# Performance work log

Measured on AMD Instinct MI355X. Metric: run time of the kernel, lower is better.

## Reference

```python
import jax, jax.numpy as jnp
import numpy as np
from jax import lax

B, N, C, NP, NS, H, L = 2, 16384, 256, 2048, 32, 4, 2
DFF = 2 * C
RADIUS = 1.0
EPS = 1e-5


def setup_inputs() -> dict:
    key = jax.random.key(0)
    ks = jax.random.split(key, 12)
    s = 0.02
    f32 = jnp.float32
    return {
        "xyz": jax.random.normal(ks[0], (B, N, 3), f32),
        "features": jax.random.normal(ks[1], (B, C, N), f32),
        # positional encoding: Conv1x1(3->C/2)+BN(eval)+ReLU, Conv1x1(C/2->C)
        "pe1_w": jax.random.normal(ks[2], (C // 2, 3), f32) * s,
        "pe1_b": jnp.zeros((C // 2,), f32),
        "bn_g": jnp.ones((C // 2,), f32),
        "bn_b": jnp.zeros((C // 2,), f32),
        "bn_m": jnp.zeros((C // 2,), f32),
        "bn_v": jnp.ones((C // 2,), f32),
        "pe2_w": jax.random.normal(ks[3], (C, C // 2), f32) * s,
        "pe2_b": jnp.zeros((C,), f32),
        # L pre-norm transformer encoder layers (stacked on leading dim)
        "ipw": jax.random.normal(ks[4], (L, 3 * C, C), f32) * s,
        "ipb": jnp.zeros((L, 3 * C), f32),
        "opw": jax.random.normal(ks[5], (L, C, C), f32) * s,
        "opb": jnp.zeros((L, C), f32),
        "ln1s": jnp.ones((L, C), f32), "ln1b": jnp.zeros((L, C), f32),
        "ln2s": jnp.ones((L, C), f32), "ln2b": jnp.zeros((L, C), f32),
        "fc1w": jax.random.normal(ks[6], (L, DFF, C), f32) * s,
        "fc1b": jnp.zeros((L, DFF), f32),
        "fc2w": jax.random.normal(ks[7], (L, C, DFF), f32) * s,
        "fc2b": jnp.zeros((L, C), f32),
    }


def _fps(xyz, npoint):
    # D-FPS starting from point 0 (pointnet2 convention). xyz: [B,N,3]
    b, n, _ = xyz.shape

    def step(carry, _):
        dists, far = carry
        centroid = jnp.take_along_axis(xyz, far[:, None, None], axis=1)  # [B,1,3]
        d = jnp.sum((xyz - centroid) ** 2, -1)
        dists = jnp.minimum(dists, d)
        return (dists, jnp.argmax(dists, -1).astype(jnp.int32)), far

    init = (jnp.full((b, n), 1e10, jnp.float32), jnp.zeros((b,), jnp.int32))
    _, idx = lax.scan(step, init, None, length=npoint)
    return idx.T  # [B, npoint]


def _ball_query(xyz, new_xyz, radius, ns):
    # first <=ns points within radius, padded with the first hit. [B,NP,NS]
    n = xyz.shape[1]
    d2 = jnp.sum((new_xyz[:, :, None, :] - xyz[:, None, :, :]) ** 2, -1)  # [B,NP,N]
    scores = jnp.where(d2 < radius * radius, jnp.arange(n, dtype=jnp.int32), n)
    svals = jnp.sort(scores, axis=-1)[..., :ns]
    order = jnp.argsort(scores, axis=-1)[..., :ns].astype(jnp.int32)
    valid = svals < n
    return jnp.where(valid, order, order[..., :1])


def _ln(x, s, b):
    m = jnp.mean(x, -1, keepdims=True)
    v = jnp.var(x, -1, keepdims=True)
    return (x - m) * lax.rsqrt(v + EPS) * s + b


def _mha(x, w, bias, ow, ob):
    # x: [S, Bn, D] (seq-first, like nn.MultiheadAttention)
    S, Bn, D = x.shape
    hd = D // H
    qkv = x @ w.T + bias
    q, k, v = jnp.split(qkv, 3, -1)
    rs = lambda t: t.reshape(S, Bn, H, hd).transpose(1, 2, 0, 3)  # [Bn,H,S,hd]
    q, k, v = rs(q), rs(k), rs(v)
    att = jax.nn.softmax(jnp.einsum('bhqd,bhkd->bhqk', q, k) * (1.0 / np.sqrt(hd)), -1)
    o = jnp.einsum('bhqk,bhkd->bhqd', att, v).transpose(2, 0, 1, 3).reshape(S, Bn, D)
    return o @ ow.T + ob


def reference(xyz, features, pe1_w, pe1_b, bn_g, bn_b, bn_m, bn_v, pe2_w, pe2_b,
              ipw, ipb, opw, opb, ln1s, ln1b, ln2s, ln2b, fc1w, fc1b, fc2w, fc2b):
    # --- sample + group ---
    fps_idx = _fps(lax.stop_gradient(xyz), NP)                       # [B,NP]
    new_xyz = jnp.take_along_axis(xyz, fps_idx[:, :, None], axis=1)  # [B,NP,3]
    idx = _ball_query(lax.stop_gradient(xyz), lax.stop_gradient(new_xyz), RADIUS, NS)
    g_xyz = jax.vmap(lambda p, i: p[i])(xyz, idx) - new_xyz[:, :, None, :]  # [B,NP,NS,3]
    g_xyz = g_xyz.transpose(0, 3, 1, 2)                              # [B,3,NP,NS]
    g_feat = jax.vmap(lambda f, i: f[:, i])(features, idx)           # [B,C,NP,NS]
    # --- positional encoding (conv1x1 + BN(eval) + ReLU, conv1x1) ---
    h = jnp.einsum('oc,bcps->bops', pe1_w, g_xyz) + pe1_b[None, :, None, None]
    h = (h - bn_m[None, :, None, None]) * lax.rsqrt(bn_v + EPS)[None, :, None, None]
    h = jax.nn.relu(h * bn_g[None, :, None, None] + bn_b[None, :, None, None])
    pe = jnp.einsum('oc,bcps->bops', pe2_w, h) + pe2_b[None, :, None, None]
    x = g_feat + pe                                                  # [B,C,NP,NS]
    # --- local transformer over each neighborhood (seq len = NS) ---
    x = x.transpose(0, 2, 1, 3).reshape(B * NP, C, NS).transpose(2, 0, 1)  # [NS,B*NP,C]
    for l in range(L):
        x = _ln(x, ln1s[l], ln1b[l])
        x = x + _mha(x, ipw[l], ipb[l], opw[l], opb[l])
        x = _ln(x, ln2s[l], ln2b[l])
        x = x + jax.nn.relu(x @ fc1w[l].T + fc1b[l]) @ fc2w[l].T + fc2b[l]
    tf = x.transpose(1, 2, 0).reshape(B, NP, C, NS).transpose(0, 2, 1, 3)  # [B,C,NP,NS]
    Lf = NP * NS

    def scat(feat_b, tf_b, idx_b):
        idx_f = idx_b.reshape(-1)          # [Lf]
        ff = tf_b.reshape(C, -1)           # [C,Lf]
        pos = jnp.arange(Lf, dtype=jnp.int32)
        first = jax.ops.segment_min(pos, idx_f, num_segments=N)  # [N], maxint if absent
        valid = first < Lf
        safe = jnp.where(valid, first, 0)
        return jnp.where(valid[None, :], ff[:, safe], feat_b)    # [C,N]

    out = jax.vmap(scat)(features, tf, idx)  # [B,C,N]
    return out.transpose(0, 2, 1)            # [B,N,C]
```

## Files before the change

### kernel.cpp

```cpp
#include <hip/hip_runtime.h>

#define NB 2
#define NN 16384
#define NC 256
#define NPp 2048
#define NSs 32
#define NH 4
#define HDh 64
#define NL 2
#define NDFF 512
#define LFv (NPp*NSs)
#define LNEPS 1e-5f
#define NBLK 256
#define NTHR 512
#define NW 8

typedef short s16x8 __attribute__((ext_vector_type(8)));
typedef float f32x4 __attribute__((ext_vector_type(4)));
typedef float f32x2 __attribute__((ext_vector_type(2)));
typedef unsigned short u16;
typedef unsigned long long u64;

struct CtlBlock { int ctr1; int ctr2; int bar; };

__device__ __forceinline__ u16 f2bf(float f){
  unsigned u = __float_as_uint(f);
  u += 0x7fffu + ((u>>16)&1u);
  return (u16)(u>>16);
}

__device__ __forceinline__ f32x4 mfma16(s16x8 a, s16x8 b, f32x4 c){
  return __builtin_amdgcn_mfma_f32_16x16x32_bf16(a, b, c, 0, 0, 0);
}

__device__ __forceinline__ f32x2 pk_add(f32x2 a, f32x2 b){
  f32x2 d; asm("v_pk_add_f32 %0, %1, %2" : "=v"(d) : "v"(a), "v"(b)); return d;
}
__device__ __forceinline__ f32x2 pk_mul(f32x2 a, f32x2 b){
  f32x2 d; asm("v_pk_mul_f32 %0, %1, %2" : "=v"(d) : "v"(a), "v"(b)); return d;
}

#define DPP_FMAX(v, ctrl) do { \
  int _iv = __float_as_int(v); \
  int _sh = __builtin_amdgcn_update_dpp(_iv, _iv, (ctrl), 0xF, 0xF, false); \
  (v) = fmaxf((v), __int_as_float(_sh)); \
} while(0)

#define DPP_IMIN(v, ctrl) do { \
  int _sh = __builtin_amdgcn_update_dpp((v), (v), (ctrl), 0xF, 0xF, false); \
  (v) = (_sh < (v)) ? _sh : (v); \
} while(0)

struct SMem {
  u64  masks[256];
  u64  keybuf[4];
  float wvc[2][NW][4];
  float cxbuf[8][4];
  float xs[32][260];
  u16  xn[32][264];
  u16  qb[32][776];
  u16  pb[NH][32][40];
  int  idx_sh[32];
  float gx_sh[32][3];
  int  misc[16];
  int  win[32];
};

__global__ void k_prep(const float* __restrict__ ipw, const float* __restrict__ opw,
                       const float* __restrict__ fc1w, const float* __restrict__ fc2w,
                       const float* __restrict__ pe2w,
                       const float* __restrict__ bng, const float* __restrict__ bnb,
                       const float* __restrict__ bnm, const float* __restrict__ bnv,
                       u16* ipwb, u16* opwb, u16* fc1wb, u16* fc2wb, u16* pe2wb,
                       float* bnsc, float* bnsh, int* first, int* rdy, CtlBlock* ctl){
  const int i0 = blockIdx.x*blockDim.x + threadIdx.x;
  const int stride = gridDim.x*blockDim.x;
  for (int i=i0; i<NL*768*NC; i+=stride) ipwb[i] = f2bf(ipw[i]);
  for (int i=i0; i<NL*NC*NC; i+=stride)  opwb[i] = f2bf(opw[i]);
  for (int i=i0; i<NL*NDFF*NC; i+=stride) fc1wb[i] = f2bf(fc1w[i]);
  for (int i=i0; i<NL*NC*NDFF; i+=stride) fc2wb[i] = f2bf(fc2w[i]);
  for (int i=i0; i<NC*128; i+=stride)    pe2wb[i] = f2bf(pe2w[i]);
  for (int i=i0; i<NB*NN; i+=stride)     first[i] = LFv;
  for (int i=i0; i<NB*NPp; i+=stride)    rdy[i] = 0;
  for (int i=i0; i<128; i+=stride){
    float sc = bng[i]*rsqrtf(bnv[i]+LNEPS);
    bnsc[i] = sc; bnsh[i] = bnb[i] - bnm[i]*sc;
  }
  if (i0 == 0){ ctl->ctr1 = 0; ctl->ctr2 = 0; ctl->bar = 0; }
}

__global__ __launch_bounds__(256) void k_featT(const float* __restrict__ feat,
                                               float* __restrict__ featT){
  __shared__ float T[32][33];
  const int b = blockIdx.y;
  const int n0 = blockIdx.x*32;
  const int t = threadIdx.x;
  const int tn = t & 31, tc = t >> 5;
  for (int cb=0; cb<NC; cb+=32){
    #pragma unroll
    for (int i=0;i<32;i+=8)
      T[tc+i][tn] = feat[((size_t)b*NC + cb+tc+i)*NN + n0+tn];
    __syncthreads();
    #pragma unroll
    for (int i=0;i<32;i+=8)
      featT[((size_t)b*NN + n0+tc+i)*NC + cb+tn] = T[tn][tc+i];
    __syncthreads();
  }
}

#define SELC(S) case S: scx = px2[(S)>>1][(S)&1]; scy = py2[(S)>>1][(S)&1]; scz = pz2[(S)>>1][(S)&1]; break;

__device__ void fps_run(int b, const float* __restrict__ xyz, u64* __restrict__ cx2,
                        int* __restrict__ rdy, SMem& sm){
#pragma clang fp contract(off)
  const int t = threadIdx.x;
  const int lane = t & 63, wid = t >> 6;
  const float* xb = xyz + (size_t)b*NN*3;
  f32x2 px2[16], py2[16], pz2[16], dd2[16];
  #pragma unroll
  for (int m=0;m<16;m++){
    int i0 = t + (2*m)*NTHR, i1 = t + (2*m+1)*NTHR;
    px2[m] = f32x2{xb[i0*3],   xb[i1*3]};
    py2[m] = f32x2{xb[i0*3+1], xb[i1*3+1]};
    pz2[m] = f32x2{xb[i0*3+2], xb[i1*3+2]};
    dd2[m] = f32x2{1e10f, 1e10f};
  }
  if (t < 4) sm.keybuf[t] = 0ull;
  float ncx, ncy, ncz;
  {
    float wx = xb[0], wy = xb[1], wz = xb[2];
    ncx=-wx; ncy=-wy; ncz=-wz;
    if (t==0){ sm.cxbuf[0][0]=wx; sm.cxbuf[0][1]=wy; sm.cxbuf[0][2]=wz; }
  }
  __syncthreads();
  for (int step=1; step<NPp; ++step){
    const f32x2 ncx2={ncx,ncx}, ncy2={ncy,ncy}, ncz2={ncz,ncz};
    float bestv = -1.f;
    #pragma unroll
    for (int m=0;m<16;m++){
      f32x2 dx = pk_add(px2[m], ncx2);
      f32x2 dy = pk_add(py2[m], ncy2);
      f32x2 dz = pk_add(pz2[m], ncz2);
      f32x2 s  = pk_add(pk_add(pk_mul(dx,dx), pk_mul(dy,dy)), pk_mul(dz,dz));
      dd2[m].x = fminf(dd2[m].x, s.x);
      dd2[m].y = fminf(dd2[m].y, s.y);
      bestv = fmaxf(fmaxf(bestv, dd2[m].x), dd2[m].y);
    }
    float M = bestv;
    DPP_FMAX(M, 0x111); DPP_FMAX(M, 0x112); DPP_FMAX(M, 0x114); DPP_FMAX(M, 0x118);
    DPP_FMAX(M, 0x142); DPP_FMAX(M, 0x143);
    const int Mi = __builtin_amdgcn_readlane(__float_as_int(M), 63);
    const float Ms = __int_as_float(Mi);
    int li = 0x7fffffff;
    #pragma unroll
    for (int m=15;m>=0;m--){
      if (dd2[m].y == Ms) li = t + (2*m+1)*NTHR;
      if (dd2[m].x == Ms) li = t + (2*m)*NTHR;
    }
    DPP_IMIN(li, 0x111); DPP_IMIN(li, 0x112); DPP_IMIN(li, 0x114); DPP_IMIN(li, 0x118);
    DPP_IMIN(li, 0x142); DPP_IMIN(li, 0x143);
    const int li63 = __builtin_amdgcn_readlane(li, 63);
    const int kb = step & 3, cb = step & 1;
    if (lane==0){
      u64 key = ((u64)(unsigned)Mi << 32) | (unsigned)(0x7fffffff - li63);
      atomicMax(&sm.keybuf[kb], key);
    }
    {
      const int slot = li63 >> 9;
      float scx=0.f, scy=0.f, scz=0.f;
      switch(slot){
        SELC(0) SELC(1) SELC(2) SELC(3) SELC(4) SELC(5) SELC(6) SELC(7)
        SELC(8) SELC(9) SELC(10) SELC(11) SELC(12) SELC(13) SELC(14) SELC(15)
        SELC(16) SELC(17) SELC(18) SELC(19) SELC(20) SELC(21) SELC(22) SELC(23)
        SELC(24) SELC(25) SELC(26) SELC(27) SELC(28) SELC(29) SELC(30) SELC(31)
        default: break;
      }
      if (t == (li63 & (NTHR-1))){
        sm.wvc[cb][wid][0]=scx; sm.wvc[cb][wid][1]=scy; sm.wvc[cb][wid][2]=scz;
      }
    }
    __syncthreads();
    const u64 kk = sm.keybuf[kb];
    const int widx = 0x7fffffff - (int)(unsigned)(kk & 0xffffffffull);
    const int wv = (widx & (NTHR-1)) >> 6;
    const float bx = sm.wvc[cb][wv][0];
    const float by = sm.wvc[cb][wv][1];
    const float bz = sm.wvc[cb][wv][2];
    ncx=-bx; ncy=-by; ncz=-bz;
    if (t==0){
      sm.cxbuf[step & 7][0]=bx; sm.cxbuf[step & 7][1]=by; sm.cxbuf[step & 7][2]=bz;
      sm.keybuf[(step+2) & 3] = 0ull;
      if ((step & 7) == 7){
        int s0 = step - 7;
        #pragma unroll
        for (int j=0;j<8;j++){
          float fx=sm.cxbuf[j][0], fy=sm.cxbuf[j][1], fz=sm.cxbuf[j][2];
          u64 lo = ((u64)__float_as_uint(fy) << 32) | __float_as_uint(fx);
          u64 hi = (u64)__float_as_uint(fz);
          size_t pb2 = (size_t)(b*NPp + s0 + j)*2;
          __hip_atomic_store(&cx2[pb2],   lo, __ATOMIC_RELAXED, __HIP_MEMORY_SCOPE_AGENT);
          __hip_atomic_store(&cx2[pb2+1], hi, __ATOMIC_RELAXED, __HIP_MEMORY_SCOPE_AGENT);
        }
        asm volatile("s_waitcnt vmcnt(0)" ::: "memory");
        #pragma unroll
        for (int j=0;j<8;j++)
          __hip_atomic_store(&rdy[b*NPp + s0 + j], 1, __ATOMIC_RELAXED, __HIP_MEMORY_SCOPE_AGENT);
      }
    }
  }
}

__device__ void seq_ballq(const float* __restrict__ xb, float cx, float cy, float cz,
                          SMem& sm, int t, int lane, int wid){
#pragma clang fp contract(off)
  for (int it=0; it<32; ++it){
    int cid = wid*32 + it;
    int i = cid*64 + lane;
    float dx=xb[i*3]-cx, dy=xb[i*3+1]-cy, dz=xb[i*3+2]-cz;
    float d2=(dx*dx+dy*dy)+dz*dz;
    u64 m = __ballot(d2 < 1.0f);
    if (lane==0) sm.masks[cid] = m;
  }
  __syncthreads();
  if (wid==0){
    u64 mk[4]; int cnt=0;
    #pragma unroll
    for (int j=0;j<4;j++){ mk[j]=sm.masks[lane*4+j]; cnt += __popcll(mk[j]); }
    int inc = cnt;
    #pragma unroll
    for (int ofs=1; ofs<64; ofs<<=1){
      int v = __shfl_up(inc, ofs);
      if (lane >= ofs) inc += v;
    }
    int r = inc - cnt;
    int tot = __shfl(inc, 63);
    #pragma unroll
    for (int j=0;j<4;j++){
      u64 msk = mk[j];
      int base = (lane*4+j)*64;
      while (msk && r < NSs){
        int bpos = __ffsll(msk)-1;
        sm.idx_sh[r] = base + bpos;
        msk &= msk-1;
        ++r;
      }
      if (r >= NSs) break;
    }
    int cc = tot < NSs ? tot : NSs;
    int pv = (tot > 0) ? sm.idx_sh[0] : 0;
    if (lane < NSs && lane >= cc) sm.idx_sh[lane] = pv;
  }
  __syncthreads();
}

__device__ __forceinline__ void ln_block512(SMem& sm, const float* __restrict__ s_,
                                            const float* __restrict__ b_, int t){
  const int s = t >> 4, j = t & 15;
  float v[16];
  float sum = 0.f;
  #pragma unroll
  for (int k=0;k<16;k++){ v[k]=sm.xs[s][j*16+k]; sum += v[k]; }
  #pragma unroll
  for (int m=1;m<16;m<<=1) sum += __shfl_xor(sum, m);
  const float mean = sum * (1.f/256.f);
  float vs = 0.f;
  #pragma unroll
  for (int k=0;k<16;k++){ float d=v[k]-mean; vs += d*d; }
  #pragma unroll
  for (int m=1;m<16;m<<=1) vs += __shfl_xor(vs, m);
  const float rstd = rsqrtf(vs*(1.f/256.f) + LNEPS);
  #pragma unroll
  for (int k=0;k<16;k++){
    int c = j*16+k;
    float y = (v[k]-mean)*rstd*s_[c] + b_[c];
    sm.xs[s][c] = y;
    sm.xn[s][c] = f2bf(y);
  }
}

__device__ void seq_pe_tf(SMem& sm, int b, float ccx, float ccy, float ccz,
    const float* __restrict__ xyz, const float* __restrict__ features,
    const float* __restrict__ featT, int useT,
    const float* __restrict__ pe1w, const float* __restrict__ pe1b,
    const float* __restrict__ bnsc, const float* __restrict__ bnsh,
    const u16* __restrict__ pe2wb, const float* __restrict__ pe2b,
    const u16* __restrict__ ipwb, const float* __restrict__ ipb,
    const u16* __restrict__ opwb, const float* __restrict__ opb,
    const float* __restrict__ ln1s, const float* __restrict__ ln1b,
    const float* __restrict__ ln2s, const float* __restrict__ ln2b,
    const u16* __restrict__ fc1wb, const float* __restrict__ fc1b,
    const u16* __restrict__ fc2wb, const float* __restrict__ fc2b){
  const int t = threadIdx.x, lane = t & 63, wid = t >> 6;
  const int c15 = lane & 15, g4 = lane >> 4;

  if (t < 96){
    int s = t/3, d = t%3;
    float cd = (d==0) ? ccx : ((d==1) ? ccy : ccz);
    sm.gx_sh[s][d] = xyz[((size_t)b*NN + sm.idx_sh[s])*3 + d] - cd;
  }
  if (useT){
    for (int e=t; e<32*NC; e+=NTHR){
      int s=e>>8, c=e&255;
      sm.xs[s][c] = featT[((size_t)b*NN + sm.idx_sh[s])*NC + c];
    }
  } else {
    for (int e=t; e<32*NC; e+=NTHR){
      int s=e>>8, c=e&255;
      sm.xs[s][c] = features[((size_t)b*NC + c)*NN + sm.idx_sh[s]];
    }
  }
  __syncthreads();
  for (int i=t; i<32*128; i+=NTHR){
    int s = i >> 7, o = i & 127;
    float h = pe1w[o*3]*sm.gx_sh[s][0] + pe1w[o*3+1]*sm.gx_sh[s][1] + pe1w[o*3+2]*sm.gx_sh[s][2] + pe1b[o];
    h = h*bnsc[o] + bnsh[o];
    sm.xn[s][o] = f2bf(h > 0.f ? h : 0.f);
  }
  __syncthreads();
  for (int tt=wid; tt<32; tt+=NW){
    int m0 = (tt & 1)*16, n0 = (tt >> 1)*16;
    f32x4 acc = {0.f,0.f,0.f,0.f};
    #pragma unroll
    for (int kk=0; kk<4; kk++){
      s16x8 a = *(const s16x8*)&sm.xn[m0+c15][kk*32 + g4*8];
      s16x8 bb = *(const s16x8*)&pe2wb[(size_t)(n0+c15)*128 + kk*32 + g4*8];
      acc = mfma16(a, bb, acc);
    }
    int col = n0 + c15;
    float bias = pe2b[col];
    #pragma unroll
    for (int r=0;r<4;r++) sm.xs[m0 + g4*4 + r][col] += acc[r] + bias;
  }
  __syncthreads();

  for (int l=0; l<NL; ++l){
    ln_block512(sm, ln1s + l*NC, ln1b + l*NC, t);
    __syncthreads();
    const u16* Wq = ipwb + (size_t)l*768*NC;
    const float* bq = ipb + l*768;
    for (int tt=wid; tt<96; tt+=NW){
      int m0 = (tt & 1)*16, n0 = (tt >> 1)*16;
      f32x4 acc = {0.f,0.f,0.f,0.f};
      #pragma unroll
      for (int kk=0;kk<8;kk++){
        s16x8 a = *(const s16x8*)&sm.xn[m0+c15][kk*32 + g4*8];
        s16x8 bb = *(const s16x8*)&Wq[(size_t)(n0+c15)*NC + kk*32 + g4*8];
        acc = mfma16(a, bb, acc);
      }
      int col = n0 + c15;
      float bias = bq[col];
      #pragma unroll
      for (int r=0;r<4;r++) sm.qb[m0 + g4*4 + r][col] = f2bf(acc[r] + bias);
    }
    __syncthreads();
    {
      const int h = wid & 3;
      const int mt = wid >> 2;
      f32x4 lac[2];
      #pragma unroll
      for (int nt=0;nt<2;nt++){
        f32x4 acc = {0.f,0.f,0.f,0.f};
        #pragma unroll
        for (int kk=0;kk<2;kk++){
          s16x8 a = *(const s16x8*)&sm.qb[mt*16+c15][h*HDh + kk*32 + g4*8];
          s16x8 bb = *(const s16x8*)&sm.qb[nt*16+c15][256 + h*HDh + kk*32 + g4*8];
          acc = mfma16(a, bb, acc);
        }
        lac[nt] = acc;
      }
      #pragma unroll
      for (int r=0;r<4;r++){
        float v0 = lac[0][r]*0.125f, v1 = lac[1][r]*0.125f;
        float mx = fmaxf(v0, v1);
        #pragma unroll
        for (int m=1;m<16;m<<=1) mx = fmaxf(mx, __shfl_xor(mx, m));
        float e0 = expf(v0-mx), e1 = expf(v1-mx);
        float smm = e0 + e1;
        #pragma unroll
        for (int m=1;m<16;m<<=1) smm += __shfl_xor(smm, m);
        float inv = 1.f/smm;
        int row = mt*16 + g4*4 + r;
        sm.pb[h][row][c15]    = f2bf(e0*inv);
        sm.pb[h][row][16+c15] = f2bf(e1*inv);
      }
      f32x4 oac[4];
      #pragma unroll
      for (int nt=0;nt<4;nt++){
        s16x8 bb;
        #pragma unroll
        for (int e=0;e<8;e++) bb[e] = (short)sm.qb[g4*8+e][512 + h*HDh + nt*16 + c15];
        f32x4 acc = {0.f,0.f,0.f,0.f};
        s16x8 a = *(const s16x8*)&sm.pb[h][mt*16+c15][g4*8];
        oac[nt] = mfma16(a, bb, acc);
      }
      __syncthreads();
      #pragma unroll
      for (int nt=0;nt<4;nt++)
        #pragma unroll
        for (int r=0;r<4;r++)
          sm.xn[mt*16 + g4*4 + r][h*HDh + nt*16 + c15] = f2bf(oac[nt][r]);
    }
    __syncthreads();
    const u16* Wo = opwb + (size_t)l*NC*NC;
    const float* bo = opb + l*NC;
    for (int tt=wid; tt<32; tt+=NW){
      int m0 = (tt & 1)*16, n0 = (tt >> 1)*16;
      f32x4 acc = {0.f,0.f,0.f,0.f};
      #pragma unroll
      for (int kk=0;kk<8;kk++){
        s16x8 a = *(const s16x8*)&sm.xn[m0+c15][kk*32 + g4*8];
        s16x8 bb = *(const s16x8*)&Wo[(size_t)(n0+c15)*NC + kk*32 + g4*8];
        acc = mfma16(a, bb, acc);
      }
      int col = n0 + c15;
      float bias = bo[col];
      #pragma unroll
      for (int r=0;r<4;r++) sm.xs[m0 + g4*4 + r][col] += acc[r] + bias;
    }
    __syncthreads();
    ln_block512(sm, ln2s + l*NC, ln2b + l*NC, t);
    __syncthreads();
    const u16* W1 = fc1wb + (size_t)l*NDFF*NC;
    for (int tt=wid; tt<64; tt+=NW){
      int m0 = (tt & 1)*16, n0 = (tt >> 1)*16;
      f32x4 acc = {0.f,0.f,0.f,0.f};
      #pragma unroll
      for (int kk=0;kk<8;kk++){
        s16x8 a = *(const s16x8*)&sm.xn[m0+c15][kk*32 + g4*8];
        s16x8 bb = *(const s16x8*)&W1[(size_t)(n0+c15)*NC + kk*32 + g4*8];
        acc = mfma16(a, bb, acc);
      }
      int col = n0 + c15;
      float bias = fc1b[l*NDFF + col];
      #pragma unroll
      for (int r=0;r<4;r++){
        float v = acc[r] + bias;
        sm.qb[m0 + g4*4 + r][col] = f2bf(v > 0.f ? v : 0.f);
      }
    }
    __syncthreads();
    const u16* W2 = fc2wb + (size_t)l*NC*NDFF;
    for (int tt=wid; tt<32; tt+=NW){
      int m0 = (tt & 1)*16, n0 = (tt >> 1)*16;
      f32x4 acc = {0.f,0.f,0.f,0.f};
      #pragma unroll
      for (int kk=0;kk<16;kk++){
        s16x8 a = *(const s16x8*)&sm.qb[m0+c15][kk*32 + g4*8];
        s16x8 bb = *(const s16x8*)&W2[(size_t)(n0+c15)*NDFF + kk*32 + g4*8];
        acc = mfma16(a, bb, acc);
      }
      int col = n0 + c15;
      float bias = fc2b[l*NC + col];
      #pragma unroll
      for (int r=0;r<4;r++) sm.xs[m0 + g4*4 + r][col] += acc[r] + bias;
    }
    __syncthreads();
  }
}

__global__ __launch_bounds__(NTHR, 2) void k_mega(
    const float* __restrict__ xyz, const float* __restrict__ features,
    const float* __restrict__ featT, int useT,
    u64* __restrict__ cx2, int* __restrict__ rdy, int* __restrict__ first, CtlBlock* ctl,
    const float* __restrict__ pe1w, const float* __restrict__ pe1b,
    const float* __restrict__ bnsc, const float* __restrict__ bnsh,
    const u16* __restrict__ pe2wb, const float* __restrict__ pe2b,
    const u16* __restrict__ ipwb, const float* __restrict__ ipb,
    const u16* __restrict__ opwb, const float* __restrict__ opb,
    const float* __restrict__ ln1s, const float* __restrict__ ln1b,
    const float* __restrict__ ln2s, const float* __restrict__ ln2b,
    const u16* __restrict__ fc1wb, const float* __restrict__ fc1b,
    const u16* __restrict__ fc2wb, const float* __restrict__ fc2b,
    float* __restrict__ out){
  __shared__ SMem sm;
  const int t = threadIdx.x, lane = t & 63, wid = t >> 6;

  if (blockIdx.x < NB){
    fps_run(blockIdx.x, xyz, cx2, rdy, sm);
  } else {
    for (;;){
      if (t==0) sm.misc[1] = atomicAdd(&ctl->ctr1, 1);
      __syncthreads();
      int p = sm.misc[1];
      if (p >= NB*NPp) break;
      int b = p >> 11, pp = p & (NPp-1);
      if (t==0){
        while (!__hip_atomic_load(&rdy[p], __ATOMIC_RELAXED, __HIP_MEMORY_SCOPE_AGENT))
          __builtin_amdgcn_s_sleep(16);
        asm volatile("" ::: "memory");
        u64 lo = __hip_atomic_load(&cx2[(size_t)p*2],   __ATOMIC_RELAXED, __HIP_MEMORY_SCOPE_AGENT);
        u64 hi = __hip_atomic_load(&cx2[(size_t)p*2+1], __ATOMIC_RELAXED, __HIP_MEMORY_SCOPE_AGENT);
        sm.misc[4] = (int)(unsigned)(lo & 0xffffffffull);
        sm.misc[5] = (int)(unsigned)(lo >> 32);
        sm.misc[6] = (int)(unsigned)(hi & 0xffffffffull);
      }
      __syncthreads();
      float cx = __int_as_float(sm.misc[4]);
      float cy = __int_as_float(sm.misc[5]);
      float cz = __int_as_float(sm.misc[6]);
      seq_ballq(xyz + (size_t)b*NN*3, cx, cy, cz, sm, t, lane, wid);
      if (t < NSs) atomicMin(&first[b*NN + sm.idx_sh[t]], pp*NSs + t);
      __syncthreads();
    }
  }

  __syncthreads();
  if (t==0){
    __builtin_amdgcn_fence(__ATOMIC_RELEASE, "agent");
    __hip_atomic_fetch_add(&ctl->bar, 1, __ATOMIC_RELAXED, __HIP_MEMORY_SCOPE_AGENT);
    while (__hip_atomic_load(&ctl->bar, __ATOMIC_RELAXED, __HIP_MEMORY_SCOPE_AGENT) < NBLK)
      __builtin_amdgcn_s_sleep(8);
    __builtin_amdgcn_fence(__ATOMIC_ACQUIRE, "agent");
  }
  __syncthreads();

  for (;;){
    if (t==0) sm.misc[1] = atomicAdd(&ctl->ctr2, 1);
    __syncthreads();
    int p = sm.misc[1];
    if (p >= NB*NPp) break;
    int b = p >> 11, pp = p & (NPp-1);
    u64 lo = cx2[(size_t)p*2], hi = cx2[(size_t)p*2+1];
    float cx = __int_as_float((int)(unsigned)(lo & 0xffffffffull));
    float cy = __int_as_float((int)(unsigned)(lo >> 32));
    float cz = __int_as_float((int)(unsigned)(hi & 0xffffffffull));
    seq_ballq(xyz + (size_t)b*NN*3, cx, cy, cz, sm, t, lane, wid);
    if (t==0) sm.misc[2] = 0;
    __syncthreads();
    if (t < NSs){
      int pos = pp*NSs + t;
      int f = first[b*NN + sm.idx_sh[t]];
      int w = (f == pos) ? 1 : 0;
      sm.win[t] = w;
      if (w) atomicOr(&sm.misc[2], 1);
    }
    __syncthreads();
    if (!sm.misc[2]) continue;
    seq_pe_tf(sm, b, cx, cy, cz, xyz, features, featT, useT,
              pe1w, pe1b, bnsc, bnsh, pe2wb, pe2b, ipwb, ipb, opwb, opb,
              ln1s, ln1b, ln2s, ln2b, fc1wb, fc1b, fc2wb, fc2b);
    for (int e=t; e<NSs*NC; e+=NTHR){
      int s = e >> 8, c = e & 255;
      if (sm.win[s]) out[((size_t)b*NN + sm.idx_sh[s])*NC + c] = sm.xs[s][c];
    }
    __syncthreads();
  }
}

__global__ __launch_bounds__(256) void k_outfill_T(const float* __restrict__ featT,
                                                   const int* __restrict__ first,
                                                   float* __restrict__ out){
  const int t = threadIdx.x;
  for (int rr=0; rr<8; ++rr){
    int row = blockIdx.x*8 + rr;
    if (first[row] == LFv)
      out[(size_t)row*NC + t] = featT[(size_t)row*NC + t];
  }
}

__global__ __launch_bounds__(256) void k_outfill_noT(const float* __restrict__ feat,
                                                     const int* __restrict__ first,
                                                     float* __restrict__ out){
  __shared__ float T[32][33];
  const int b = blockIdx.y;
  const int n0 = blockIdx.x*32;
  const int t = threadIdx.x;
  const int tn = t & 31, tc = t >> 5;
  for (int cb=0; cb<NC; cb+=32){
    #pragma unroll
    for (int i=0;i<32;i+=8)
      T[tc+i][tn] = feat[((size_t)b*NC + cb+tc+i)*NN + n0+tn];
    __syncthreads();
    #pragma unroll
    for (int i=0;i<32;i+=8){
      int n = n0 + tc + i;
      if (first[b*NN+n] == LFv)
        out[((size_t)b*NN + n)*NC + cb+tn] = T[tn][tc+i];
    }
    __syncthreads();
  }
}

extern "C" void kernel_launch(void* const* d_in, const int* in_sizes, int n_in,
                              void* d_out, int out_size, void* d_ws, size_t ws_size,
                              hipStream_t stream){
  const float* xyz   = (const float*)d_in[0];
  const float* feat  = (const float*)d_in[1];
  const float* pe1w  = (const float*)d_in[2];
  const float* pe1b  = (const float*)d_in[3];
  const float* bng   = (const float*)d_in[4];
  const float* bnb   = (const float*)d_in[5];
  const float* bnm   = (const float*)d_in[6];
  const float* bnv   = (const float*)d_in[7];
  const float* pe2w  = (const float*)d_in[8];
  const float* pe2b  = (const float*)d_in[9];
  const float* ipw   = (const float*)d_in[10];
  const float* ipb   = (const float*)d_in[11];
  const float* opw   = (const float*)d_in[12];
  const float* opb   = (const float*)d_in[13];
  const float* ln1s  = (const float*)d_in[14];
  const float* ln1b  = (const float*)d_in[15];
  const float* ln2s  = (const float*)d_in[16];
  const float* ln2b  = (const float*)d_in[17];
  const float* fc1w  = (const float*)d_in[18];
  const float* fc1b  = (const float*)d_in[19];
  const float* fc2w  = (const float*)d_in[20];
  const float* fc2b  = (const float*)d_in[21];
  float* out = (float*)d_out;

  char* ws = (char*)d_ws;
  size_t off = 0;
  auto alloc = [&](size_t bytes)->void*{
    void* p = ws + off;
    off = (off + bytes + 255) & ~(size_t)255;
    return p;
  };
  u64*   cx2     = (u64*)  alloc((size_t)NB*NPp*2*8);
  int*   rdy     = (int*)  alloc((size_t)NB*NPp*4);
  int*   first   = (int*)  alloc((size_t)NB*NN*4);
  CtlBlock* ctl  = (CtlBlock*)alloc(sizeof(CtlBlock));
  float* bnsc    = (float*)alloc(128*4);
  float* bnsh    = (float*)alloc(128*4);
  u16*   ipwb    = (u16*)  alloc((size_t)NL*768*NC*2);
  u16*   opwb    = (u16*)  alloc((size_t)NL*NC*NC*2);
  u16*   fc1wb   = (u16*)  alloc((size_t)NL*NDFF*NC*2);
  u16*   fc2wb   = (u16*)  alloc((size_t)NL*NC*NDFF*2);
  u16*   pe2wb   = (u16*)  alloc((size_t)NC*128*2);
  int useT = (off + (size_t)NB*NN*NC*4 <= ws_size) ? 1 : 0;
  float* featT = (float*)(useT ? alloc((size_t)NB*NN*NC*4) : (void*)ws);

  k_prep<<<512, 256, 0, stream>>>(ipw, opw, fc1w, fc2w, pe2w, bng, bnb, bnm, bnv,
                                  ipwb, opwb, fc1wb, fc2wb, pe2wb, bnsc, bnsh,
                                  first, rdy, ctl);
  if (useT)
    k_featT<<<dim3(NN/32, NB), 256, 0, stream>>>(feat, featT);

  const float* featT_c = featT;
  void* kargs[] = {
    (void*)&xyz, (void*)&feat, (void*)&featT_c, (void*)&useT,
    (void*)&cx2, (void*)&rdy, (void*)&first, (void*)&ctl,
    (void*)&pe1w, (void*)&pe1b, (void*)&bnsc, (void*)&bnsh,
    (void*)&pe2wb, (void*)&pe2b, (void*)&ipwb, (void*)&ipb,
    (void*)&opwb, (void*)&opb, (void*)&ln1s, (void*)&ln1b,
    (void*)&ln2s, (void*)&ln2b, (void*)&fc1wb, (void*)&fc1b,
    (void*)&fc2wb, (void*)&fc2b, (void*)&out };
  hipLaunchCooperativeKernel((void*)k_mega, dim3(NBLK), dim3(NTHR), kargs, 0, stream);

  if (useT)
    k_outfill_T<<<(NB*NN)/8, 256, 0, stream>>>(featT, first, out);
  else
    k_outfill_noT<<<dim3(NN/32, NB), 256, 0, stream>>>(feat, first, out);
  (void)in_sizes; (void)n_in; (void)out_size;
}
```

Before: 4.693 ms.

## Split FPS per batch across four cooperating blocks with cross-block argmax exchange

Farthest-point sampling for each batch now runs on four blocks, each owning a quarter of the points, instead of one block. Each step every block computes a local max key and writes it to tagged global slots, then spins on its peers' slots to agree on the global winner. The per-step wave argmin reduction becomes ballot/ffs, and centroids are published each step with a tag word instead of in batches of eight with a ready flag. Ball-query indices are saved to global memory so the second phase reuses them instead of recomputing the query. The risk is that per-step global spin-synchronisation latency between blocks may outweigh the smaller per-block work, and the extra FPS blocks take workers away from the ball-query pool.

```diff
diff --git a/kernel.cpp b/kernel.cpp
--- a/kernel.cpp
+++ b/kernel.cpp
@@ -14,6 +14,8 @@
 #define NBLK 256
 #define NTHR 512
 #define NW 8
+#define NQ 4
+#define CHUNK (NN/NQ)
 
 typedef short s16x8 __attribute__((ext_vector_type(8)));
 typedef float f32x4 __attribute__((ext_vector_type(4)));
@@ -46,16 +48,10 @@
   (v) = fmaxf((v), __int_as_float(_sh)); \
 } while(0)
 
-#define DPP_IMIN(v, ctrl) do { \
-  int _sh = __builtin_amdgcn_update_dpp((v), (v), (ctrl), 0xF, 0xF, false); \
-  (v) = (_sh < (v)) ? _sh : (v); \
-} while(0)
-
 struct SMem {
   u64  masks[256];
   u64  keybuf[4];
   float wvc[2][NW][4];
-  float cxbuf[8][4];
   float xs[32][260];
   u16  xn[32][264];
   u16  qb[32][776];
@@ -72,7 +68,8 @@
                        const float* __restrict__ bng, const float* __restrict__ bnb,
                        const float* __restrict__ bnm, const float* __restrict__ bnv,
                        u16* ipwb, u16* opwb, u16* fc1wb, u16* fc2wb, u16* pe2wb,
-                       float* bnsc, float* bnsh, int* first, int* rdy, CtlBlock* ctl){
+                       float* bnsc, float* bnsh, int* first, u64* cx2, u64* slots,
+                       CtlBlock* ctl){
   const int i0 = blockIdx.x*blockDim.x + threadIdx.x;
   const int stride = gridDim.x*blockDim.x;
   for (int i=i0; i<NL*768*NC; i+=stride) ipwb[i] = f2bf(ipw[i]);
@@ -81,7 +78,8 @@
   for (int i=i0; i<NL*NC*NDFF; i+=stride) fc2wb[i] = f2bf(fc2w[i]);
   for (int i=i0; i<NC*128; i+=stride)    pe2wb[i] = f2bf(pe2w[i]);
   for (int i=i0; i<NB*NN; i+=stride)     first[i] = LFv;
-  for (int i=i0; i<NB*NPp; i+=stride)    rdy[i] = 0;
+  for (int i=i0; i<NB*NPp*3; i+=stride)  cx2[i] = 0ull;
+  for (int i=i0; i<NB*NQ*2*5; i+=stride) slots[i] = 0ull;
   for (int i=i0; i<128; i+=stride){
     float sc = bng[i]*rsqrtf(bnv[i]+LNEPS);
     bnsc[i] = sc; bnsh[i] = bnb[i] - bnm[i]*sc;
@@ -110,16 +108,18 @@
 
 #define SELC(S) case S: scx = px2[(S)>>1][(S)&1]; scy = py2[(S)>>1][(S)&1]; scz = pz2[(S)>>1][(S)&1]; break;
 
-__device__ void fps_run(int b, const float* __restrict__ xyz, u64* __restrict__ cx2,
-                        int* __restrict__ rdy, SMem& sm){
+__device__ void fps_run4(int b, int q, const float* __restrict__ xyz,
+                         u64* __restrict__ cx2, u64* __restrict__ slots, SMem& sm){
 #pragma clang fp contract(off)
   const int t = threadIdx.x;
   const int lane = t & 63, wid = t >> 6;
+  const int wbase = wid*64;
   const float* xb = xyz + (size_t)b*NN*3;
-  f32x2 px2[16], py2[16], pz2[16], dd2[16];
+  const int gbase = q*CHUNK;
+  f32x2 px2[4], py2[4], pz2[4], dd2[4];
   #pragma unroll
-  for (int m=0;m<16;m++){
-    int i0 = t + (2*m)*NTHR, i1 = t + (2*m+1)*NTHR;
+  for (int m=0;m<4;m++){
+    int i0 = gbase + t + (2*m)*NTHR, i1 = gbase + t + (2*m+1)*NTHR;
     px2[m] = f32x2{xb[i0*3],   xb[i1*3]};
     py2[m] = f32x2{xb[i0*3+1], xb[i1*3+1]};
     pz2[m] = f32x2{xb[i0*3+2], xb[i1*3+2]};
@@ -130,14 +130,19 @@
   {
     float wx = xb[0], wy = xb[1], wz = xb[2];
     ncx=-wx; ncy=-wy; ncz=-wz;
-    if (t==0){ sm.cxbuf[0][0]=wx; sm.cxbuf[0][1]=wy; sm.cxbuf[0][2]=wz; }
+    if (t==0 && q==0){
+      size_t p0 = (size_t)(b*NPp)*3;
+      __hip_atomic_store(&cx2[p0+0], ((u64)__float_as_uint(wx)<<32)|1u, __ATOMIC_RELAXED, __HIP_MEMORY_SCOPE_AGENT);
+      __hip_atomic_store(&cx2[p0+1], ((u64)__float_as_uint(wy)<<32)|1u, __ATOMIC_RELAXED, __HIP_MEMORY_SCOPE_AGENT);
+      __hip_atomic_store(&cx2[p0+2], ((u64)__float_as_uint(wz)<<32)|1u, __ATOMIC_RELAXED, __HIP_MEMORY_SCOPE_AGENT);
+    }
   }
   __syncthreads();
   for (int step=1; step<NPp; ++step){
     const f32x2 ncx2={ncx,ncx}, ncy2={ncy,ncy}, ncz2={ncz,ncz};
     float bestv = -1.f;
     #pragma unroll
-    for (int m=0;m<16;m++){
+    for (int m=0;m<4;m++){
       f32x2 dx = pk_add(px2[m], ncx2);
       f32x2 dy = pk_add(py2[m], ncy2);
       f32x2 dz = pk_add(pz2[m], ncz2);
@@ -151,62 +156,91 @@
     DPP_FMAX(M, 0x142); DPP_FMAX(M, 0x143);
     const int Mi = __builtin_amdgcn_readlane(__float_as_int(M), 63);
     const float Ms = __int_as_float(Mi);
-    int li = 0x7fffffff;
-    #pragma unroll
-    for (int m=15;m>=0;m--){
-      if (dd2[m].y == Ms) li = t + (2*m+1)*NTHR;
-      if (dd2[m].x == Ms) li = t + (2*m)*NTHR;
-    }
-    DPP_IMIN(li, 0x111); DPP_IMIN(li, 0x112); DPP_IMIN(li, 0x114); DPP_IMIN(li, 0x118);
-    DPP_IMIN(li, 0x142); DPP_IMIN(li, 0x143);
-    const int li63 = __builtin_amdgcn_readlane(li, 63);
+    u64 bs[8];
+    #pragma unroll
+    for (int m=0;m<4;m++){
+      bs[2*m]   = __ballot(dd2[m].x == Ms);
+      bs[2*m+1] = __ballot(dd2[m].y == Ms);
+    }
+    int lc = 0;
+    #pragma unroll
+    for (int s=7;s>=0;s--)
+      if (bs[s]) lc = wbase + s*NTHR + (__ffsll(bs[s])-1);
     const int kb = step & 3, cb = step & 1;
     if (lane==0){
-      u64 key = ((u64)(unsigned)Mi << 32) | (unsigned)(0x7fffffff - li63);
+      u64 key = ((u64)(unsigned)Mi << 32) | (unsigned)(0x7fffffff - (gbase + lc));
       atomicMax(&sm.keybuf[kb], key);
     }
     {
-      const int slot = li63 >> 9;
+      const int slot = lc >> 9;
       float scx=0.f, scy=0.f, scz=0.f;
       switch(slot){
         SELC(0) SELC(1) SELC(2) SELC(3) SELC(4) SELC(5) SELC(6) SELC(7)
-        SELC(8) SELC(9) SELC(10) SELC(11) SELC(12) SELC(13) SELC(14) SELC(15)
-        SELC(16) SELC(17) SELC(18) SELC(19) SELC(20) SELC(21) SELC(22) SELC(23)
-        SELC(24) SELC(25) SELC(26) SELC(27) SELC(28) SELC(29) SELC(30) SELC(31)
         default: break;
       }
-      if (t == (li63 & (NTHR-1))){
+      if (t == (lc & (NTHR-1))){
         sm.wvc[cb][wid][0]=scx; sm.wvc[cb][wid][1]=scy; sm.wvc[cb][wid][2]=scz;
       }
     }
     __syncthreads();
-    const u64 kk = sm.keybuf[kb];
-    const int widx = 0x7fffffff - (int)(unsigned)(kk & 0xffffffffull);
-    const int wv = (widx & (NTHR-1)) >> 6;
-    const float bx = sm.wvc[cb][wv][0];
-    const float by = sm.wvc[cb][wv][1];
-    const float bz = sm.wvc[cb][wv][2];
-    ncx=-bx; ncy=-by; ncz=-bz;
-    if (t==0){
-      sm.cxbuf[step & 7][0]=bx; sm.cxbuf[step & 7][1]=by; sm.cxbuf[step & 7][2]=bz;
-      sm.keybuf[(step+2) & 3] = 0ull;
-      if ((step & 7) == 7){
-        int s0 = step - 7;
-        #pragma unroll
-        for (int j=0;j<8;j++){
-          float fx=sm.cxbuf[j][0], fy=sm.cxbuf[j][1], fz=sm.cxbuf[j][2];
-          u64 lo = ((u64)__float_as_uint(fy) << 32) | __float_as_uint(fx);
-          u64 hi = (u64)__float_as_uint(fz);
-          size_t pb2 = (size_t)(b*NPp + s0 + j)*2;
-          __hip_atomic_store(&cx2[pb2],   lo, __ATOMIC_RELAXED, __HIP_MEMORY_SCOPE_AGENT);
-          __hip_atomic_store(&cx2[pb2+1], hi, __ATOMIC_RELAXED, __HIP_MEMORY_SCOPE_AGENT);
+    if (wid==0){
+      const u64 kloc = sm.keybuf[kb];
+      const int gidx = 0x7fffffff - (int)(unsigned)(kloc & 0xffffffffull);
+      const int wv = ((gidx - gbase) & (NTHR-1)) >> 6;
+      const float bx = sm.wvc[cb][wv][0];
+      const float by = sm.wvc[cb][wv][1];
+      const float bz = sm.wvc[cb][wv][2];
+      const unsigned tag = (unsigned)step;
+      u64 w0 = (kloc & 0xffffffff00000000ull) | tag;
+      u64 w1 = ((kloc & 0xffffffffull) << 32) | tag;
+      u64 w2 = ((u64)__float_as_uint(bx) << 32) | tag;
+      u64 w3 = ((u64)__float_as_uint(by) << 32) | tag;
+      u64 w4 = ((u64)__float_as_uint(bz) << 32) | tag;
+      u64 wown = (lane==0)?w0 : (lane==1)?w1 : (lane==2)?w2 : (lane==3)?w3 : w4;
+      u64* mybase = slots + (size_t)(((b*NQ + q)*2 + cb)*5);
+      if (lane < 5)
+        __hip_atomic_store(&mybase[lane], wown, __ATOMIC_RELAXED, __HIP_MEMORY_SCOPE_AGENT);
+      unsigned vhi = 0;
+      if (lane < 15){
+        int pi = lane/5, wj = lane - pi*5;
+        int peerq = pi + (pi >= q ? 1 : 0);
+        u64* src = slots + (size_t)(((b*NQ + peerq)*2 + cb)*5 + wj);
+        u64 v;
+        do { v = __hip_atomic_load(src, __ATOMIC_RELAXED, __HIP_MEMORY_SCOPE_AGENT); }
+        while ((unsigned)v != tag);
+        vhi = (unsigned)(v >> 32);
+      }
+      u64 bk = kloc;
+      unsigned fxb = __float_as_uint(bx), fyb = __float_as_uint(by), fzb = __float_as_uint(bz);
+      #pragma unroll
+      for (int pi=0; pi<3; pi++){
+        unsigned mh = (unsigned)__builtin_amdgcn_readlane((int)vhi, pi*5+0);
+        unsigned il = (unsigned)__builtin_amdgcn_readlane((int)vhi, pi*5+1);
+        u64 kp = ((u64)mh << 32) | il;
+        if (kp > bk){
+          bk = kp;
+          fxb = (unsigned)__builtin_amdgcn_readlane((int)vhi, pi*5+2);
+          fyb = (unsigned)__builtin_amdgcn_readlane((int)vhi, pi*5+3);
+          fzb = (unsigned)__builtin_amdgcn_readlane((int)vhi, pi*5+4);
         }
-        asm volatile("s_waitcnt vmcnt(0)" ::: "memory");
-        #pragma unroll
-        for (int j=0;j<8;j++)
-          __hip_atomic_store(&rdy[b*NPp + s0 + j], 1, __ATOMIC_RELAXED, __HIP_MEMORY_SCOPE_AGENT);
-      }
-    }
+      }
+      if (lane==0){
+        sm.misc[8]  = (int)fxb;
+        sm.misc[9]  = (int)fyb;
+        sm.misc[10] = (int)fzb;
+        sm.keybuf[(step+2) & 3] = 0ull;
+        if (q==0){
+          size_t pb3 = (size_t)(b*NPp + step)*3;
+          __hip_atomic_store(&cx2[pb3+0], ((u64)fxb<<32)|1u, __ATOMIC_RELAXED, __HIP_MEMORY_SCOPE_AGENT);
+          __hip_atomic_store(&cx2[pb3+1], ((u64)fyb<<32)|1u, __ATOMIC_RELAXED, __HIP_MEMORY_SCOPE_AGENT);
+          __hip_atomic_store(&cx2[pb3+2], ((u64)fzb<<32)|1u, __ATOMIC_RELAXED, __HIP_MEMORY_SCOPE_AGENT);
+        }
+      }
+    }
+    __syncthreads();
+    ncx = -__int_as_float(sm.misc[8]);
+    ncy = -__int_as_float(sm.misc[9]);
+    ncz = -__int_as_float(sm.misc[10]);
   }
 }
 
@@ -461,7 +495,8 @@
 __global__ __launch_bounds__(NTHR, 2) void k_mega(
     const float* __restrict__ xyz, const float* __restrict__ features,
     const float* __restrict__ featT, int useT,
-    u64* __restrict__ cx2, int* __restrict__ rdy, int* __restrict__ first, CtlBlock* ctl,
+    u64* __restrict__ cx2, u64* __restrict__ slots, int* __restrict__ idxg,
+    int* __restrict__ first, CtlBlock* ctl,
     const float* __restrict__ pe1w, const float* __restrict__ pe1b,
     const float* __restrict__ bnsc, const float* __restrict__ bnsh,
     const u16* __restrict__ pe2wb, const float* __restrict__ pe2b,
@@ -474,9 +509,12 @@
     float* __restrict__ out){
   __shared__ SMem sm;
   const int t = threadIdx.x, lane = t & 63, wid = t >> 6;
-
-  if (blockIdx.x < NB){
-    fps_run(blockIdx.x, xyz, cx2, rdy, sm);
+  const int bid = blockIdx.x;
+  const int r8 = bid & 7;
+  const bool isfps = (r8 < NB) && (bid < NQ*8);
+
+  if (isfps){
+    fps_run4(r8, bid >> 3, xyz, cx2, slots, sm);
   } else {
     for (;;){
       if (t==0) sm.misc[1] = atomicAdd(&ctl->ctr1, 1);
@@ -485,21 +523,26 @@
       if (p >= NB*NPp) break;
       int b = p >> 11, pp = p & (NPp-1);
       if (t==0){
-        while (!__hip_atomic_load(&rdy[p], __ATOMIC_RELAXED, __HIP_MEMORY_SCOPE_AGENT))
-          __builtin_amdgcn_s_sleep(16);
-        asm volatile("" ::: "memory");
-        u64 lo = __hip_atomic_load(&cx2[(size_t)p*2],   __ATOMIC_RELAXED, __HIP_MEMORY_SCOPE_AGENT);
-        u64 hi = __hip_atomic_load(&cx2[(size_t)p*2+1], __ATOMIC_RELAXED, __HIP_MEMORY_SCOPE_AGENT);
-        sm.misc[4] = (int)(unsigned)(lo & 0xffffffffull);
-        sm.misc[5] = (int)(unsigned)(lo >> 32);
-        sm.misc[6] = (int)(unsigned)(hi & 0xffffffffull);
+        const u64* w = &cx2[(size_t)p*3];
+        u64 w0, w1, w2;
+        do { w0 = __hip_atomic_load(&w[0], __ATOMIC_RELAXED, __HIP_MEMORY_SCOPE_AGENT);
+             if ((unsigned)w0 != 1u) __builtin_amdgcn_s_sleep(4);
+        } while ((unsigned)w0 != 1u);
+        do { w1 = __hip_atomic_load(&w[1], __ATOMIC_RELAXED, __HIP_MEMORY_SCOPE_AGENT); } while ((unsigned)w1 != 1u);
+        do { w2 = __hip_atomic_load(&w[2], __ATOMIC_RELAXED, __HIP_MEMORY_SCOPE_AGENT); } while ((unsigned)w2 != 1u);
+        sm.misc[4] = (int)(unsigned)(w0 >> 32);
+        sm.misc[5] = (int)(unsigned)(w1 >> 32);
+        sm.misc[6] = (int)(unsigned)(w2 >> 32);
       }
       __syncthreads();
       float cx = __int_as_float(sm.misc[4]);
       float cy = __int_as_float(sm.misc[5]);
       float cz = __int_as_float(sm.misc[6]);
       seq_ballq(xyz + (size_t)b*NN*3, cx, cy, cz, sm, t, lane, wid);
-      if (t < NSs) atomicMin(&first[b*NN + sm.idx_sh[t]], pp*NSs + t);
+      if (t < NSs){
+        atomicMin(&first[b*NN + sm.idx_sh[t]], pp*NSs + t);
+        idxg[(size_t)p*NSs + t] = sm.idx_sh[t];
+      }
       __syncthreads();
     }
   }
@@ -520,11 +563,7 @@
     int p = sm.misc[1];
     if (p >= NB*NPp) break;
     int b = p >> 11, pp = p & (NPp-1);
-    u64 lo = cx2[(size_t)p*2], hi = cx2[(size_t)p*2+1];
-    float cx = __int_as_float((int)(unsigned)(lo & 0xffffffffull));
-    float cy = __int_as_float((int)(unsigned)(lo >> 32));
-    float cz = __int_as_float((int)(unsigned)(hi & 0xffffffffull));
-    seq_ballq(xyz + (size_t)b*NN*3, cx, cy, cz, sm, t, lane, wid);
+    if (t < NSs) sm.idx_sh[t] = idxg[(size_t)p*NSs + t];
     if (t==0) sm.misc[2] = 0;
     __syncthreads();
     if (t < NSs){
@@ -536,6 +575,10 @@
     }
     __syncthreads();
     if (!sm.misc[2]) continue;
+    u64 w0 = cx2[(size_t)p*3], w1 = cx2[(size_t)p*3+1], w2 = cx2[(size_t)p*3+2];
+    float cx = __int_as_float((int)(unsigned)(w0 >> 32));
+    float cy = __int_as_float((int)(unsigned)(w1 >> 32));
+    float cz = __int_as_float((int)(unsigned)(w2 >> 32));
     seq_pe_tf(sm, b, cx, cy, cz, xyz, features, featT, useT,
               pe1w, pe1b, bnsc, bnsh, pe2wb, pe2b, ipwb, ipb, opwb, opb,
               ln1s, ln1b, ln2s, ln2b, fc1wb, fc1b, fc2wb, fc2b);
@@ -615,8 +658,9 @@
     off = (off + bytes + 255) & ~(size_t)255;
     return p;
   };
-  u64*   cx2     = (u64*)  alloc((size_t)NB*NPp*2*8);
-  int*   rdy     = (int*)  alloc((size_t)NB*NPp*4);
+  u64*   cx2     = (u64*)  alloc((size_t)NB*NPp*3*8);
+  u64*   slots   = (u64*)  alloc((size_t)NB*NQ*2*5*8);
+  int*   idxg    = (int*)  alloc((size_t)NB*NPp*NSs*4);
   int*   first   = (int*)  alloc((size_t)NB*NN*4);
   CtlBlock* ctl  = (CtlBlock*)alloc(sizeof(CtlBlock));
   float* bnsc    = (float*)alloc(128*4);
@@ -631,14 +675,14 @@
 
   k_prep<<<512, 256, 0, stream>>>(ipw, opw, fc1w, fc2w, pe2w, bng, bnb, bnm, bnv,
                                   ipwb, opwb, fc1wb, fc2wb, pe2wb, bnsc, bnsh,
-                                  first, rdy, ctl);
+                                  first, cx2, slots, ctl);
   if (useT)
     k_featT<<<dim3(NN/32, NB), 256, 0, stream>>>(feat, featT);
 
   const float* featT_c = featT;
   void* kargs[] = {
     (void*)&xyz, (void*)&feat, (void*)&featT_c, (void*)&useT,
-    (void*)&cx2, (void*)&rdy, (void*)&first, (void*)&ctl,
+    (void*)&cx2, (void*)&slots, (void*)&idxg, (void*)&first, (void*)&ctl,
     (void*)&pe1w, (void*)&pe1b, (void*)&bnsc, (void*)&bnsh,
     (void*)&pe2wb, (void*)&pe2b, (void*)&ipwb, (void*)&ipb,
     (void*)&opwb, (void*)&opb, (void*)&ln1s, (void*)&ln1b,
```

New measurement: 4.839 ms. 1.03x slower.
